# Performance work log

Measured on AMD Instinct MI355X. Metric: run time of the kernel, lower is better.

## Reference

```python
import jax, jax.numpy as jnp
import numpy as np

N, E = 50000, 800000
IN_F, HID, OUT, HEADS = 128, 64, 128, 4
NEG_SLOPE = 0.2


def setup_inputs() -> dict:
    key = jax.random.key(0)
    ks = jax.random.split(key, 10)
    s = 0.05
    return {
        "x": jax.random.normal(ks[0], (N, IN_F), dtype=jnp.float32),
        "edge_index": jax.random.randint(ks[1], (2, E), 0, N, dtype=jnp.int64),
        "W1": jax.random.normal(ks[2], (IN_F, HEADS * HID), dtype=jnp.float32) * s,
        "att_src1": jax.random.normal(ks[3], (HEADS, HID), dtype=jnp.float32) * s,
        "att_dst1": jax.random.normal(ks[4], (HEADS, HID), dtype=jnp.float32) * s,
        "b1": jnp.zeros((HEADS * HID,), dtype=jnp.float32),
        "W2": jax.random.normal(ks[5], (HEADS * HID, OUT), dtype=jnp.float32) * s,
        "att_src2": jax.random.normal(ks[6], (1, OUT), dtype=jnp.float32) * s,
        "att_dst2": jax.random.normal(ks[7], (1, OUT), dtype=jnp.float32) * s,
        "b2": jnp.zeros((OUT,), dtype=jnp.float32),
    }


def _gat_layer(x, W, a_src, a_dst, b, src, dst, heads, out_c):
    n = x.shape[0]
    h = (x @ W).reshape(n, heads, out_c)              # [N, H, C]
    alpha_s = jnp.einsum("nhc,hc->nh", h, a_src)       # [N, H]
    alpha_d = jnp.einsum("nhc,hc->nh", h, a_dst)
    e = jax.nn.leaky_relu(alpha_s[src] + alpha_d[dst], NEG_SLOPE)  # [E, H]
    # scatter-softmax over edges grouped by destination node
    m = jax.ops.segment_max(e, dst, num_segments=n)
    ex = jnp.exp(e - m[dst])
    denom = jax.ops.segment_sum(ex, dst, num_segments=n)
    alpha = ex / denom[dst]                            # [E, H]
    out = jax.ops.segment_sum(alpha[:, :, None] * h[src], dst, num_segments=n)
    return out.reshape(n, heads * out_c) + b


def reference(x, edge_index, W1, att_src1, att_dst1, b1, W2, att_src2, att_dst2, b2):
    n = x.shape[0]
    loop = jnp.arange(n, dtype=edge_index.dtype)       # PyG add_self_loops=True
    src = jnp.concatenate([edge_index[0], loop])
    dst = jnp.concatenate([edge_index[1], loop])
    h = _gat_layer(x, W1, att_src1, att_dst1, b1, src, dst, HEADS, HID)
    h = jax.nn.elu(h)
    out = _gat_layer(h, W2, att_src2, att_dst2, b2, src, dst, 1, OUT)
    return out
```

## Files before the change

kernel.cpp:

```cpp
#include <hip/hip_runtime.h>
#include <hip/hip_bf16.h>

#define NEG_SLOPE 0.2f

typedef short bf16x8 __attribute__((ext_vector_type(8)));
typedef float f32x4 __attribute__((ext_vector_type(4)));

__device__ __forceinline__ float bf2f(unsigned short u) {
    return __uint_as_float(((unsigned int)u) << 16);
}
__device__ __forceinline__ unsigned short f2bf(float f) {
    unsigned int x = __float_as_uint(f);
    unsigned int lsb = (x >> 16) & 1u;
    x += 0x7fffu + lsb;
    return (unsigned short)(x >> 16);
}


__global__ void cast_x_kernel(const float* __restrict__ x, unsigned short* __restrict__ xb,
                              int n4) {
    int i = blockIdx.x * 256 + threadIdx.x;
    if (i >= n4) return;
    float4 v = *(const float4*)(x + (size_t)i * 4);
    ushort4 b;
    b.x = f2bf(v.x); b.y = f2bf(v.y); b.z = f2bf(v.z); b.w = f2bf(v.w);
    *(ushort4*)(xb + (size_t)i * 4) = b;
}

__global__ void cast_w_kernel(const float* __restrict__ W, unsigned short* __restrict__ Wt,
                              int K, int NC) {
    int idx = blockIdx.x * 256 + threadIdx.x;
    if (idx >= K * NC) return;
    int k = idx / NC, n = idx % NC;
    Wt[(size_t)n * K + k] = f2bf(W[idx]);
}


__global__ void degree_kernel(const int* __restrict__ ei, int E, int N,
                              int* __restrict__ deg) {
    int e = blockIdx.x * blockDim.x + threadIdx.x;
    int EA = E + N;
    if (e >= EA) return;
    int dst = (e < E) ? ei[E + e] : (e - E);
    atomicAdd(&deg[dst], 1);
}

__global__ void scan_local(const int* __restrict__ deg, int* __restrict__ offs,
                           int* __restrict__ bsum, int N) {
    __shared__ int wsum[16];
    int tid = threadIdx.x;
    int lane = tid & 63;
    int wave = tid >> 6;
    int i = blockIdx.x * 1024 + tid;
    int v = (i < N) ? deg[i] : 0;
    int x = v;
    #pragma unroll
    for (int off = 1; off < 64; off <<= 1) {
        int t = __shfl_up(x, off);
        if (lane >= off) x += t;
    }
    if (lane == 63) wsum[wave] = x;
    __syncthreads();
    if (wave == 0 && lane < 16) {
        int w = wsum[lane];
        #pragma unroll
        for (int off = 1; off < 16; off <<= 1) {
            int t = __shfl_up(w, off);
            if (lane >= off) w += t;
        }
        wsum[lane] = w;
    }
    __syncthreads();
    int wexcl = (wave > 0) ? wsum[wave - 1] : 0;
    if (i <= N) offs[i] = wexcl + x - v;
    if (tid == 0) bsum[blockIdx.x] = wsum[15];
}

__global__ void scan_bsums(int* __restrict__ bsum, int nb) {
    __shared__ int wsum[16];
    int tid = threadIdx.x;
    int lane = tid & 63;
    int wave = tid >> 6;
    int v = (tid < nb) ? bsum[tid] : 0;
    int x = v;
    #pragma unroll
    for (int off = 1; off < 64; off <<= 1) {
        int t = __shfl_up(x, off);
        if (lane >= off) x += t;
    }
    if (lane == 63) wsum[wave] = x;
    __syncthreads();
    if (wave == 0 && lane < 16) {
        int w = wsum[lane];
        #pragma unroll
        for (int off = 1; off < 16; off <<= 1) {
            int t = __shfl_up(w, off);
            if (lane >= off) w += t;
        }
        wsum[lane] = w;
    }
    __syncthreads();
    int wexcl = (wave > 0) ? wsum[wave - 1] : 0;
    if (tid < nb) bsum[tid] = wexcl + x - v;
}

__global__ void scan_add(int* __restrict__ offs, const int* __restrict__ bsum, int N) {
    int i = blockIdx.x * 1024 + threadIdx.x;
    if (i <= N) offs[i] += bsum[blockIdx.x];
}

__global__ void scatter_kernel(const int* __restrict__ ei, int E, int N,
                               const int* __restrict__ offs, int* __restrict__ cnt,
                               int* __restrict__ col) {
    int e = blockIdx.x * blockDim.x + threadIdx.x;
    int EA = E + N;
    if (e >= EA) return;
    int s, d;
    if (e < E) { s = ei[e]; d = ei[E + e]; }
    else       { s = d = e - E; }
    int pos = offs[d] + atomicAdd(&cnt[d], 1);
    col[pos] = s;
}

__global__ void gemm1_mfma(const unsigned short* __restrict__ Ab,
                           const unsigned short* __restrict__ Wt,
                           unsigned short* __restrict__ hb, int M) {
    int wave = threadIdx.x >> 6;
    int lane = threadIdx.x & 63;
    int quad = lane >> 4;
    int l16 = lane & 15;
    int m0 = blockIdx.x * 64 + wave * 16;
    int rowc = min(m0 + l16, M - 1);
    bf16x8 a[4];
    const unsigned short* ap = Ab + (size_t)rowc * 128 + quad * 8;
    #pragma unroll
    for (int kc = 0; kc < 4; ++kc) a[kc] = *(const bf16x8*)(ap + kc * 32);
    f32x4 acc[16];
    #pragma unroll
    for (int nt = 0; nt < 16; ++nt) {
        f32x4 c = {0.f, 0.f, 0.f, 0.f};
        const unsigned short* bp = Wt + (size_t)(nt * 16 + l16) * 128 + quad * 8;
        #pragma unroll
        for (int kc = 0; kc < 4; ++kc) {
            bf16x8 b = *(const bf16x8*)(bp + kc * 32);
            c = __builtin_amdgcn_mfma_f32_16x16x32_bf16(a[kc], b, c, 0, 0, 0);
        }
        acc[nt] = c;
    }
    int srow0 = m0 + quad * 4;
    #pragma unroll
    for (int r = 0; r < 4; ++r) {
        int srow = srow0 + r;
        if (srow < M) {
            #pragma unroll
            for (int nt = 0; nt < 16; ++nt)
                hb[(size_t)srow * 256 + nt * 16 + l16] = f2bf(acc[nt][r]);
        }
    }
}

__global__ void gemm2_mfma(const unsigned short* __restrict__ Ab,
                           const unsigned short* __restrict__ Wt,
                           unsigned short* __restrict__ hb, int M) {
    int wave = threadIdx.x >> 6;
    int lane = threadIdx.x & 63;
    int quad = lane >> 4;
    int l16 = lane & 15;
    int m0 = blockIdx.x * 64 + wave * 16;
    int rowc = min(m0 + l16, M - 1);
    bf16x8 a[8];
    const unsigned short* ap = Ab + (size_t)rowc * 256 + quad * 8;
    #pragma unroll
    for (int kc = 0; kc < 8; ++kc) a[kc] = *(const bf16x8*)(ap + kc * 32);
    f32x4 acc[8];
    #pragma unroll
    for (int nt = 0; nt < 8; ++nt) {
        f32x4 c = {0.f, 0.f, 0.f, 0.f};
        const unsigned short* bp = Wt + (size_t)(nt * 16 + l16) * 256 + quad * 8;
        #pragma unroll
        for (int kc = 0; kc < 8; ++kc) {
            bf16x8 b = *(const bf16x8*)(bp + kc * 32);
            c = __builtin_amdgcn_mfma_f32_16x16x32_bf16(a[kc], b, c, 0, 0, 0);
        }
        acc[nt] = c;
    }
    int srow0 = m0 + quad * 4;
    #pragma unroll
    for (int r = 0; r < 4; ++r) {
        int srow = srow0 + r;
        if (srow < M) {
            #pragma unroll
            for (int nt = 0; nt < 8; ++nt)
                hb[(size_t)srow * 128 + nt * 16 + l16] = f2bf(acc[nt][r]);
        }
    }
}

__global__ void alpha1_kernel(const unsigned short* __restrict__ hb,
                              const float* __restrict__ att_s,
                              const float* __restrict__ att_d,
                              float* __restrict__ as, float* __restrict__ ad, int N) {
    int node = blockIdx.x * 4 + (threadIdx.x >> 6);
    if (node >= N) return;
    int lane = threadIdx.x & 63;
    int c0 = lane * 4;
    uint2 g = *(const uint2*)(hb + (size_t)node * 256 + c0);
    float h0 = __uint_as_float(g.x << 16);
    float h1 = __uint_as_float(g.x & 0xffff0000u);
    float h2 = __uint_as_float(g.y << 16);
    float h3 = __uint_as_float(g.y & 0xffff0000u);
    float4 sv = *(const float4*)(att_s + c0);
    float4 dv = *(const float4*)(att_d + c0);
    float ps = h0 * sv.x + h1 * sv.y + h2 * sv.z + h3 * sv.w;
    float pd = h0 * dv.x + h1 * dv.y + h2 * dv.z + h3 * dv.w;
    #pragma unroll
    for (int off = 1; off < 16; off <<= 1) {
        ps += __shfl_xor(ps, off);
        pd += __shfl_xor(pd, off);
    }
    if ((lane & 15) == 0) {
        int head = lane >> 4;
        as[node * 4 + head] = ps;
        ad[node * 4 + head] = pd;
    }
}

__global__ void alpha2_kernel(const unsigned short* __restrict__ hb,
                              const float* __restrict__ att_s,
                              const float* __restrict__ att_d,
                              float* __restrict__ as, float* __restrict__ ad, int N) {
    int node = blockIdx.x * 4 + (threadIdx.x >> 6);
    if (node >= N) return;
    int lane = threadIdx.x & 63;
    int c0 = lane * 2;
    unsigned int g = *(const unsigned int*)(hb + (size_t)node * 128 + c0);
    float h0 = __uint_as_float(g << 16);
    float h1 = __uint_as_float(g & 0xffff0000u);
    float2 sv = *(const float2*)(att_s + c0);
    float2 dv = *(const float2*)(att_d + c0);
    float ps = h0 * sv.x + h1 * sv.y;
    float pd = h0 * dv.x + h1 * dv.y;
    #pragma unroll
    for (int off = 1; off < 64; off <<= 1) {
        ps += __shfl_xor(ps, off);
        pd += __shfl_xor(pd, off);
    }
    if (lane == 0) { as[node] = ps; ad[node] = pd; }
}

__global__ void agg1_kernel(const unsigned short* __restrict__ hb,
                            const float* __restrict__ as,
                            const float* __restrict__ ad,
                            const int* __restrict__ offs, const int* __restrict__ col,
                            const float* __restrict__ b1,
                            unsigned short* __restrict__ out, int N) {
    int node = blockIdx.x * 4 + (threadIdx.x >> 6);
    if (node >= N) return;
    int lane = threadIdx.x & 63;
    int half = lane >> 5;
    int sub  = lane & 31;
    int head = sub >> 3;
    int c0 = sub * 8;
    float adv = ad[node * 4 + head];
    int beg = offs[node], end = offs[node + 1];
    float d = 0.f;
    float acc[8] = {};
    int j = beg + half;
    for (; j + 2 < end; j += 4) {
        int s0 = col[j];
        int s1 = col[j + 2];
        uint4 g0 = *(const uint4*)(hb + (size_t)s0 * 256 + c0);
        uint4 g1 = *(const uint4*)(hb + (size_t)s1 * 256 + c0);
        float e0 = as[s0 * 4 + head] + adv;
        float e1 = as[s1 * 4 + head] + adv;
        e0 = (e0 > 0.f) ? e0 : NEG_SLOPE * e0;
        e1 = (e1 > 0.f) ? e1 : NEG_SLOPE * e1;
        float p0 = __expf(e0);
        float p1 = __expf(e1);
        d += p0 + p1;
        const unsigned int* w0 = (const unsigned int*)&g0;
        const unsigned int* w1 = (const unsigned int*)&g1;
        #pragma unroll
        for (int i = 0; i < 4; ++i) {
            acc[2 * i]     = fmaf(p0, __uint_as_float(w0[i] << 16), acc[2 * i]);
            acc[2 * i + 1] = fmaf(p0, __uint_as_float(w0[i] & 0xffff0000u), acc[2 * i + 1]);
            acc[2 * i]     = fmaf(p1, __uint_as_float(w1[i] << 16), acc[2 * i]);
            acc[2 * i + 1] = fmaf(p1, __uint_as_float(w1[i] & 0xffff0000u), acc[2 * i + 1]);
        }
    }
    for (; j < end; j += 2) {
        int s = col[j];
        uint4 g = *(const uint4*)(hb + (size_t)s * 256 + c0);
        float e = as[s * 4 + head] + adv;
        e = (e > 0.f) ? e : NEG_SLOPE * e;
        float p = __expf(e);
        d += p;
        const unsigned int* w = (const unsigned int*)&g;
        #pragma unroll
        for (int i = 0; i < 4; ++i) {
            acc[2 * i]     = fmaf(p, __uint_as_float(w[i] << 16), acc[2 * i]);
            acc[2 * i + 1] = fmaf(p, __uint_as_float(w[i] & 0xffff0000u), acc[2 * i + 1]);
        }
    }
    d += __shfl_xor(d, 32);
    #pragma unroll
    for (int i = 0; i < 8; ++i) acc[i] += __shfl_xor(acc[i], 32);
    if (half == 0) {
        float inv = 1.f / d;
        float4 bb0 = *(const float4*)(b1 + c0);
        float4 bb1 = *(const float4*)(b1 + c0 + 4);
        float bb[8] = {bb0.x, bb0.y, bb0.z, bb0.w, bb1.x, bb1.y, bb1.z, bb1.w};
        unsigned short o[8];
        #pragma unroll
        for (int i = 0; i < 8; ++i) {
            float v = acc[i] * inv + bb[i];
            v = (v > 0.f) ? v : (__expf(v) - 1.f);
            o[i] = f2bf(v);
        }
        ushort4 p0 = {o[0], o[1], o[2], o[3]};
        ushort4 p1 = {o[4], o[5], o[6], o[7]};
        *(ushort4*)(out + (size_t)node * 256 + c0) = p0;
        *(ushort4*)(out + (size_t)node * 256 + c0 + 4) = p1;
    }
}

__global__ void agg2_kernel(const unsigned short* __restrict__ hb,
                            const float* __restrict__ as,
                            const float* __restrict__ ad,
                            const int* __restrict__ offs, const int* __restrict__ col,
                            const float* __restrict__ b2,
                            float* __restrict__ out, int N) {
    int node = blockIdx.x * 4 + (threadIdx.x >> 6);
    if (node >= N) return;
    int lane = threadIdx.x & 63;
    int q   = lane >> 4;
    int sub = lane & 15;
    int c0 = sub * 8;
    float adv = ad[node];
    int beg = offs[node], end = offs[node + 1];
    float d = 0.f;
    float acc[8] = {};
    int j = beg + q;
    for (; j + 4 < end; j += 8) {
        int s0 = col[j];
        int s1 = col[j + 4];
        uint4 g0 = *(const uint4*)(hb + (size_t)s0 * 128 + c0);
        uint4 g1 = *(const uint4*)(hb + (size_t)s1 * 128 + c0);
        float e0 = as[s0] + adv;
        float e1 = as[s1] + adv;
        e0 = (e0 > 0.f) ? e0 : NEG_SLOPE * e0;
        e1 = (e1 > 0.f) ? e1 : NEG_SLOPE * e1;
        float p0 = __expf(e0);
        float p1 = __expf(e1);
        d += p0 + p1;
        const unsigned int* w0 = (const unsigned int*)&g0;
        const unsigned int* w1 = (const unsigned int*)&g1;
        #pragma unroll
        for (int i = 0; i < 4; ++i) {
            acc[2 * i]     = fmaf(p0, __uint_as_float(w0[i] << 16), acc[2 * i]);
            acc[2 * i + 1] = fmaf(p0, __uint_as_float(w0[i] & 0xffff0000u), acc[2 * i + 1]);
            acc[2 * i]     = fmaf(p1, __uint_as_float(w1[i] << 16), acc[2 * i]);
            acc[2 * i + 1] = fmaf(p1, __uint_as_float(w1[i] & 0xffff0000u), acc[2 * i + 1]);
        }
    }
    for (; j < end; j += 4) {
        int s = col[j];
        uint4 g = *(const uint4*)(hb + (size_t)s * 128 + c0);
        float e = as[s] + adv;
        e = (e > 0.f) ? e : NEG_SLOPE * e;
        float p = __expf(e);
        d += p;
        const unsigned int* w = (const unsigned int*)&g;
        #pragma unroll
        for (int i = 0; i < 4; ++i) {
            acc[2 * i]     = fmaf(p, __uint_as_float(w[i] << 16), acc[2 * i]);
            acc[2 * i + 1] = fmaf(p, __uint_as_float(w[i] & 0xffff0000u), acc[2 * i + 1]);
        }
    }
    d += __shfl_xor(d, 16);
    d += __shfl_xor(d, 32);
    #pragma unroll
    for (int i = 0; i < 8; ++i) {
        acc[i] += __shfl_xor(acc[i], 16);
        acc[i] += __shfl_xor(acc[i], 32);
    }
    if (lane < 16) {
        float inv = 1.f / d;
        float4 bb0 = *(const float4*)(b2 + c0);
        float4 bb1 = *(const float4*)(b2 + c0 + 4);
        float bb[8] = {bb0.x, bb0.y, bb0.z, bb0.w, bb1.x, bb1.y, bb1.z, bb1.w};
        float o[8];
        #pragma unroll
        for (int i = 0; i < 8; ++i) o[i] = acc[i] * inv + bb[i];
        *(float4*)(out + (size_t)node * 128 + c0) = make_float4(o[0], o[1], o[2], o[3]);
        *(float4*)(out + (size_t)node * 128 + c0 + 4) = make_float4(o[4], o[5], o[6], o[7]);
    }
}


extern "C" void kernel_launch(void* const* d_in, const int* in_sizes, int n_in,
                              void* d_out, int out_size, void* d_ws, size_t ws_size,
                              hipStream_t stream) {
    const float* x    = (const float*)d_in[0];
    const int*   ei   = (const int*)d_in[1];
    const float* W1   = (const float*)d_in[2];
    const float* at_s1 = (const float*)d_in[3];
    const float* at_d1 = (const float*)d_in[4];
    const float* b1   = (const float*)d_in[5];
    const float* W2   = (const float*)d_in[6];
    const float* at_s2 = (const float*)d_in[7];
    const float* at_d2 = (const float*)d_in[8];
    const float* b2   = (const float*)d_in[9];
    float* out = (float*)d_out;

    const int N  = in_sizes[0] / 128;
    const int E  = in_sizes[1] / 2;
    const int EA = E + N;

    char* ws = (char*)d_ws;
    size_t off = 0;
    auto alloc = [&](size_t bytes) -> void* {
        void* p = ws + off;
        off += (bytes + 255) & ~(size_t)255;
        return p;
    };
    unsigned short* xb   = (unsigned short*)alloc((size_t)N * 128 * 2);
    unsigned short* wt1  = (unsigned short*)alloc((size_t)256 * 128 * 2);
    unsigned short* wt2  = (unsigned short*)alloc((size_t)128 * 256 * 2);
    unsigned short* h1b  = (unsigned short*)alloc((size_t)N * 256 * 2);
    unsigned short* h1ab = (unsigned short*)alloc((size_t)N * 256 * 2);
    unsigned short* h2b  = (unsigned short*)alloc((size_t)N * 128 * 2);
    float* as1 = (float*)alloc((size_t)N * 4 * 4);
    float* ad1 = (float*)alloc((size_t)N * 4 * 4);
    float* as2 = (float*)alloc((size_t)N * 4);
    float* ad2 = (float*)alloc((size_t)N * 4);
    int* deg  = (int*)alloc((size_t)2 * N * 4);
    int* cnt  = deg + N;
    int* offs = (int*)alloc((size_t)(N + 1) * 4);
    int* bsum = (int*)alloc((size_t)1024 * 4);
    int* col  = (int*)alloc((size_t)EA * 4);

    const int nb = (N + 1 + 1023) / 1024;

    hipMemsetAsync(deg, 0, (size_t)2 * N * 4, stream);
    cast_x_kernel<<<(N * 128 / 4 + 255) / 256, 256, 0, stream>>>(x, xb, N * 128 / 4);
    cast_w_kernel<<<(128 * 256 + 255) / 256, 256, 0, stream>>>(W1, wt1, 128, 256);
    cast_w_kernel<<<(256 * 128 + 255) / 256, 256, 0, stream>>>(W2, wt2, 256, 128);
    degree_kernel<<<(EA + 255) / 256, 256, 0, stream>>>(ei, E, N, deg);
    scan_local<<<nb, 1024, 0, stream>>>(deg, offs, bsum, N);
    scan_bsums<<<1, 1024, 0, stream>>>(bsum, nb);
    scan_add<<<nb, 1024, 0, stream>>>(offs, bsum, N);
    scatter_kernel<<<(EA + 255) / 256, 256, 0, stream>>>(ei, E, N, offs, cnt, col);

    gemm1_mfma<<<(N + 63) / 64, 256, 0, stream>>>(xb, wt1, h1b, N);
    alpha1_kernel<<<(N + 3) / 4, 256, 0, stream>>>(h1b, at_s1, at_d1, as1, ad1, N);
    agg1_kernel<<<(N + 3) / 4, 256, 0, stream>>>(h1b, as1, ad1, offs, col, b1, h1ab, N);

    gemm2_mfma<<<(N + 63) / 64, 256, 0, stream>>>(h1ab, wt2, h2b, N);
    alpha2_kernel<<<(N + 3) / 4, 256, 0, stream>>>(h2b, at_s2, at_d2, as2, ad2, N);
    agg2_kernel<<<(N + 3) / 4, 256, 0, stream>>>(h2b, as2, ad2, offs, col, b2, out, N);
}
```

Baseline: 371.5 us.

## Fuse x cast and attention-score dots into GEMM epilogues; unroll aggregation

```diff
diff --git a/kernel.cpp b/kernel.cpp
--- a/kernel.cpp
+++ b/kernel.cpp
@@ -5,6 +5,7 @@
 
 typedef short bf16x8 __attribute__((ext_vector_type(8)));
 typedef float f32x4 __attribute__((ext_vector_type(4)));
+typedef float f32x2 __attribute__((ext_vector_type(2)));
 
 __device__ __forceinline__ float bf2f(unsigned short u) {
     return __uint_as_float(((unsigned int)u) << 16);
@@ -15,16 +16,11 @@
     x += 0x7fffu + lsb;
     return (unsigned short)(x >> 16);
 }
-
-
-__global__ void cast_x_kernel(const float* __restrict__ x, unsigned short* __restrict__ xb,
-                              int n4) {
-    int i = blockIdx.x * 256 + threadIdx.x;
-    if (i >= n4) return;
-    float4 v = *(const float4*)(x + (size_t)i * 4);
-    ushort4 b;
-    b.x = f2bf(v.x); b.y = f2bf(v.y); b.z = f2bf(v.z); b.w = f2bf(v.w);
-    *(ushort4*)(xb + (size_t)i * 4) = b;
+__device__ __forceinline__ f32x2 upk(unsigned int u) {
+    f32x2 r;
+    r.x = __uint_as_float(u << 16);
+    r.y = __uint_as_float(u & 0xffff0000u);
+    return r;
 }
 
 __global__ void cast_w_kernel(const float* __restrict__ W, unsigned short* __restrict__ Wt,
@@ -122,9 +118,11 @@
     col[pos] = s;
 }
 
-__global__ void gemm1_mfma(const unsigned short* __restrict__ Ab,
+__global__ void gemm1_mfma(const float* __restrict__ A,
                            const unsigned short* __restrict__ Wt,
-                           unsigned short* __restrict__ hb, int M) {
+                           const float* __restrict__ att_s, const float* __restrict__ att_d,
+                           unsigned short* __restrict__ hb,
+                           float* __restrict__ as, float* __restrict__ ad, int M) {
     int wave = threadIdx.x >> 6;
     int lane = threadIdx.x & 63;
     int quad = lane >> 4;
@@ -132,9 +130,18 @@
     int m0 = blockIdx.x * 64 + wave * 16;
     int rowc = min(m0 + l16, M - 1);
     bf16x8 a[4];
-    const unsigned short* ap = Ab + (size_t)rowc * 128 + quad * 8;
-    #pragma unroll
-    for (int kc = 0; kc < 4; ++kc) a[kc] = *(const bf16x8*)(ap + kc * 32);
+    const float* ap = A + (size_t)rowc * 128 + quad * 8;
+    #pragma unroll
+    for (int kc = 0; kc < 4; ++kc) {
+        float4 f0 = *(const float4*)(ap + kc * 32);
+        float4 f1 = *(const float4*)(ap + kc * 32 + 4);
+        bf16x8 v;
+        v[0] = (short)f2bf(f0.x); v[1] = (short)f2bf(f0.y);
+        v[2] = (short)f2bf(f0.z); v[3] = (short)f2bf(f0.w);
+        v[4] = (short)f2bf(f1.x); v[5] = (short)f2bf(f1.y);
+        v[6] = (short)f2bf(f1.z); v[7] = (short)f2bf(f1.w);
+        a[kc] = v;
+    }
     f32x4 acc[16];
     #pragma unroll
     for (int nt = 0; nt < 16; ++nt) {
@@ -147,21 +154,46 @@
         }
         acc[nt] = c;
     }
+    float asv[16], adv[16];
+    #pragma unroll
+    for (int nt = 0; nt < 16; ++nt) {
+        asv[nt] = att_s[nt * 16 + l16];
+        adv[nt] = att_d[nt * 16 + l16];
+    }
     int srow0 = m0 + quad * 4;
     #pragma unroll
     for (int r = 0; r < 4; ++r) {
         int srow = srow0 + r;
-        if (srow < M) {
+        bool ok = srow < M;
+        if (ok) {
             #pragma unroll
             for (int nt = 0; nt < 16; ++nt)
                 hb[(size_t)srow * 256 + nt * 16 + l16] = f2bf(acc[nt][r]);
         }
+        #pragma unroll
+        for (int h = 0; h < 4; ++h) {
+            float ps = acc[4 * h][r] * asv[4 * h] + acc[4 * h + 1][r] * asv[4 * h + 1]
+                     + acc[4 * h + 2][r] * asv[4 * h + 2] + acc[4 * h + 3][r] * asv[4 * h + 3];
+            float pd = acc[4 * h][r] * adv[4 * h] + acc[4 * h + 1][r] * adv[4 * h + 1]
+                     + acc[4 * h + 2][r] * adv[4 * h + 2] + acc[4 * h + 3][r] * adv[4 * h + 3];
+            #pragma unroll
+            for (int off = 1; off < 16; off <<= 1) {
+                ps += __shfl_xor(ps, off);
+                pd += __shfl_xor(pd, off);
+            }
+            if (ok && l16 == 0) {
+                as[srow * 4 + h] = ps;
+                ad[srow * 4 + h] = pd;
+            }
+        }
     }
 }
 
 __global__ void gemm2_mfma(const unsigned short* __restrict__ Ab,
                            const unsigned short* __restrict__ Wt,
-                           unsigned short* __restrict__ hb, int M) {
+                           const float* __restrict__ att_s, const float* __restrict__ att_d,
+                           unsigned short* __restrict__ hb,
+                           float* __restrict__ as, float* __restrict__ ad, int M) {
     int wave = threadIdx.x >> 6;
     int lane = threadIdx.x & 63;
     int quad = lane >> 4;
@@ -184,68 +216,35 @@
         }
         acc[nt] = c;
     }
+    float asv[8], adv[8];
+    #pragma unroll
+    for (int nt = 0; nt < 8; ++nt) {
+        asv[nt] = att_s[nt * 16 + l16];
+        adv[nt] = att_d[nt * 16 + l16];
+    }
     int srow0 = m0 + quad * 4;
     #pragma unroll
     for (int r = 0; r < 4; ++r) {
         int srow = srow0 + r;
-        if (srow < M) {
+        bool ok = srow < M;
+        if (ok) {
             #pragma unroll
             for (int nt = 0; nt < 8; ++nt)
                 hb[(size_t)srow * 128 + nt * 16 + l16] = f2bf(acc[nt][r]);
         }
-    }
-}
-
-__global__ void alpha1_kernel(const unsigned short* __restrict__ hb,
-                              const float* __restrict__ att_s,
-                              const float* __restrict__ att_d,
-                              float* __restrict__ as, float* __restrict__ ad, int N) {
-    int node = blockIdx.x * 4 + (threadIdx.x >> 6);
-    if (node >= N) return;
-    int lane = threadIdx.x & 63;
-    int c0 = lane * 4;
-    uint2 g = *(const uint2*)(hb + (size_t)node * 256 + c0);
-    float h0 = __uint_as_float(g.x << 16);
-    float h1 = __uint_as_float(g.x & 0xffff0000u);
-    float h2 = __uint_as_float(g.y << 16);
-    float h3 = __uint_as_float(g.y & 0xffff0000u);
-    float4 sv = *(const float4*)(att_s + c0);
-    float4 dv = *(const float4*)(att_d + c0);
-    float ps = h0 * sv.x + h1 * sv.y + h2 * sv.z + h3 * sv.w;
-    float pd = h0 * dv.x + h1 * dv.y + h2 * dv.z + h3 * dv.w;
-    #pragma unroll
-    for (int off = 1; off < 16; off <<= 1) {
-        ps += __shfl_xor(ps, off);
-        pd += __shfl_xor(pd, off);
-    }
-    if ((lane & 15) == 0) {
-        int head = lane >> 4;
-        as[node * 4 + head] = ps;
-        ad[node * 4 + head] = pd;
-    }
-}
-
-__global__ void alpha2_kernel(const unsigned short* __restrict__ hb,
-                              const float* __restrict__ att_s,
-                              const float* __restrict__ att_d,
-                              float* __restrict__ as, float* __restrict__ ad, int N) {
-    int node = blockIdx.x * 4 + (threadIdx.x >> 6);
-    if (node >= N) return;
-    int lane = threadIdx.x & 63;
-    int c0 = lane * 2;
-    unsigned int g = *(const unsigned int*)(hb + (size_t)node * 128 + c0);
-    float h0 = __uint_as_float(g << 16);
-    float h1 = __uint_as_float(g & 0xffff0000u);
-    float2 sv = *(const float2*)(att_s + c0);
-    float2 dv = *(const float2*)(att_d + c0);
-    float ps = h0 * sv.x + h1 * sv.y;
-    float pd = h0 * dv.x + h1 * dv.y;
-    #pragma unroll
-    for (int off = 1; off < 64; off <<= 1) {
-        ps += __shfl_xor(ps, off);
-        pd += __shfl_xor(pd, off);
-    }
-    if (lane == 0) { as[node] = ps; ad[node] = pd; }
+        float ps = 0.f, pd = 0.f;
+        #pragma unroll
+        for (int nt = 0; nt < 8; ++nt) {
+            ps = fmaf(acc[nt][r], asv[nt], ps);
+            pd = fmaf(acc[nt][r], adv[nt], pd);
+        }
+        #pragma unroll
+        for (int off = 1; off < 16; off <<= 1) {
+            ps += __shfl_xor(ps, off);
+            pd += __shfl_xor(pd, off);
+        }
+        if (ok && l16 == 0) { as[srow] = ps; ad[srow] = pd; }
+    }
 }
 
 __global__ void agg1_kernel(const unsigned short* __restrict__ hb,
@@ -264,8 +263,40 @@
     float adv = ad[node * 4 + head];
     int beg = offs[node], end = offs[node + 1];
     float d = 0.f;
-    float acc[8] = {};
+    f32x2 acc[4] = {};
     int j = beg + half;
+    for (; j + 6 < end; j += 8) {
+        int s0 = col[j];
+        int s1 = col[j + 2];
+        int s2 = col[j + 4];
+        int s3 = col[j + 6];
+        uint4 g0 = *(const uint4*)(hb + (size_t)s0 * 256 + c0);
+        uint4 g1 = *(const uint4*)(hb + (size_t)s1 * 256 + c0);
+        uint4 g2 = *(const uint4*)(hb + (size_t)s2 * 256 + c0);
+        uint4 g3 = *(const uint4*)(hb + (size_t)s3 * 256 + c0);
+        float e0 = as[s0 * 4 + head] + adv;
+        float e1 = as[s1 * 4 + head] + adv;
+        float e2 = as[s2 * 4 + head] + adv;
+        float e3 = as[s3 * 4 + head] + adv;
+        e0 = (e0 > 0.f) ? e0 : NEG_SLOPE * e0;
+        e1 = (e1 > 0.f) ? e1 : NEG_SLOPE * e1;
+        e2 = (e2 > 0.f) ? e2 : NEG_SLOPE * e2;
+        e3 = (e3 > 0.f) ? e3 : NEG_SLOPE * e3;
+        float p0 = __expf(e0), p1 = __expf(e1), p2 = __expf(e2), p3 = __expf(e3);
+        d += (p0 + p1) + (p2 + p3);
+        const unsigned int* w0 = (const unsigned int*)&g0;
+        const unsigned int* w1 = (const unsigned int*)&g1;
+        const unsigned int* w2 = (const unsigned int*)&g2;
+        const unsigned int* w3 = (const unsigned int*)&g3;
+        f32x2 v0 = {p0, p0}, v1 = {p1, p1}, v2 = {p2, p2}, v3 = {p3, p3};
+        #pragma unroll
+        for (int i = 0; i < 4; ++i) {
+            acc[i] = __builtin_elementwise_fma(v0, upk(w0[i]), acc[i]);
+            acc[i] = __builtin_elementwise_fma(v1, upk(w1[i]), acc[i]);
+            acc[i] = __builtin_elementwise_fma(v2, upk(w2[i]), acc[i]);
+            acc[i] = __builtin_elementwise_fma(v3, upk(w3[i]), acc[i]);
+        }
+    }
     for (; j + 2 < end; j += 4) {
         int s0 = col[j];
         int s1 = col[j + 2];
@@ -275,17 +306,15 @@
         float e1 = as[s1 * 4 + head] + adv;
         e0 = (e0 > 0.f) ? e0 : NEG_SLOPE * e0;
         e1 = (e1 > 0.f) ? e1 : NEG_SLOPE * e1;
-        float p0 = __expf(e0);
-        float p1 = __expf(e1);
+        float p0 = __expf(e0), p1 = __expf(e1);
         d += p0 + p1;
         const unsigned int* w0 = (const unsigned int*)&g0;
         const unsigned int* w1 = (const unsigned int*)&g1;
+        f32x2 v0 = {p0, p0}, v1 = {p1, p1};
         #pragma unroll
         for (int i = 0; i < 4; ++i) {
-            acc[2 * i]     = fmaf(p0, __uint_as_float(w0[i] << 16), acc[2 * i]);
-            acc[2 * i + 1] = fmaf(p0, __uint_as_float(w0[i] & 0xffff0000u), acc[2 * i + 1]);
-            acc[2 * i]     = fmaf(p1, __uint_as_float(w1[i] << 16), acc[2 * i]);
-            acc[2 * i + 1] = fmaf(p1, __uint_as_float(w1[i] & 0xffff0000u), acc[2 * i + 1]);
+            acc[i] = __builtin_elementwise_fma(v0, upk(w0[i]), acc[i]);
+            acc[i] = __builtin_elementwise_fma(v1, upk(w1[i]), acc[i]);
         }
     }
     for (; j < end; j += 2) {
@@ -296,24 +325,28 @@
         float p = __expf(e);
         d += p;
         const unsigned int* w = (const unsigned int*)&g;
-        #pragma unroll
-        for (int i = 0; i < 4; ++i) {
-            acc[2 * i]     = fmaf(p, __uint_as_float(w[i] << 16), acc[2 * i]);
-            acc[2 * i + 1] = fmaf(p, __uint_as_float(w[i] & 0xffff0000u), acc[2 * i + 1]);
-        }
+        f32x2 v = {p, p};
+        #pragma unroll
+        for (int i = 0; i < 4; ++i)
+            acc[i] = __builtin_elementwise_fma(v, upk(w[i]), acc[i]);
     }
     d += __shfl_xor(d, 32);
     #pragma unroll
-    for (int i = 0; i < 8; ++i) acc[i] += __shfl_xor(acc[i], 32);
+    for (int i = 0; i < 4; ++i) {
+        acc[i].x += __shfl_xor(acc[i].x, 32);
+        acc[i].y += __shfl_xor(acc[i].y, 32);
+    }
     if (half == 0) {
         float inv = 1.f / d;
         float4 bb0 = *(const float4*)(b1 + c0);
         float4 bb1 = *(const float4*)(b1 + c0 + 4);
+        float av[8] = {acc[0].x, acc[0].y, acc[1].x, acc[1].y,
+                       acc[2].x, acc[2].y, acc[3].x, acc[3].y};
         float bb[8] = {bb0.x, bb0.y, bb0.z, bb0.w, bb1.x, bb1.y, bb1.z, bb1.w};
         unsigned short o[8];
         #pragma unroll
         for (int i = 0; i < 8; ++i) {
-            float v = acc[i] * inv + bb[i];
+            float v = av[i] * inv + bb[i];
             v = (v > 0.f) ? v : (__expf(v) - 1.f);
             o[i] = f2bf(v);
         }
@@ -339,7 +372,7 @@
     float adv = ad[node];
     int beg = offs[node], end = offs[node + 1];
     float d = 0.f;
-    float acc[8] = {};
+    f32x2 acc[4] = {};
     int j = beg + q;
     for (; j + 4 < end; j += 8) {
         int s0 = col[j];
@@ -350,17 +383,15 @@
         float e1 = as[s1] + adv;
         e0 = (e0 > 0.f) ? e0 : NEG_SLOPE * e0;
         e1 = (e1 > 0.f) ? e1 : NEG_SLOPE * e1;
-        float p0 = __expf(e0);
-        float p1 = __expf(e1);
+        float p0 = __expf(e0), p1 = __expf(e1);
         d += p0 + p1;
         const unsigned int* w0 = (const unsigned int*)&g0;
         const unsigned int* w1 = (const unsigned int*)&g1;
+        f32x2 v0 = {p0, p0}, v1 = {p1, p1};
         #pragma unroll
         for (int i = 0; i < 4; ++i) {
-            acc[2 * i]     = fmaf(p0, __uint_as_float(w0[i] << 16), acc[2 * i]);
-            acc[2 * i + 1] = fmaf(p0, __uint_as_float(w0[i] & 0xffff0000u), acc[2 * i + 1]);
-            acc[2 * i]     = fmaf(p1, __uint_as_float(w1[i] << 16), acc[2 * i]);
-            acc[2 * i + 1] = fmaf(p1, __uint_as_float(w1[i] & 0xffff0000u), acc[2 * i + 1]);
+            acc[i] = __builtin_elementwise_fma(v0, upk(w0[i]), acc[i]);
+            acc[i] = __builtin_elementwise_fma(v1, upk(w1[i]), acc[i]);
         }
     }
     for (; j < end; j += 4) {
@@ -371,27 +402,30 @@
         float p = __expf(e);
         d += p;
         const unsigned int* w = (const unsigned int*)&g;
-        #pragma unroll
-        for (int i = 0; i < 4; ++i) {
-            acc[2 * i]     = fmaf(p, __uint_as_float(w[i] << 16), acc[2 * i]);
-            acc[2 * i + 1] = fmaf(p, __uint_as_float(w[i] & 0xffff0000u), acc[2 * i + 1]);
-        }
+        f32x2 v = {p, p};
+        #pragma unroll
+        for (int i = 0; i < 4; ++i)
+            acc[i] = __builtin_elementwise_fma(v, upk(w[i]), acc[i]);
     }
     d += __shfl_xor(d, 16);
     d += __shfl_xor(d, 32);
     #pragma unroll
-    for (int i = 0; i < 8; ++i) {
-        acc[i] += __shfl_xor(acc[i], 16);
-        acc[i] += __shfl_xor(acc[i], 32);
+    for (int i = 0; i < 4; ++i) {
+        acc[i].x += __shfl_xor(acc[i].x, 16);
+        acc[i].x += __shfl_xor(acc[i].x, 32);
+        acc[i].y += __shfl_xor(acc[i].y, 16);
+        acc[i].y += __shfl_xor(acc[i].y, 32);
     }
     if (lane < 16) {
         float inv = 1.f / d;
         float4 bb0 = *(const float4*)(b2 + c0);
         float4 bb1 = *(const float4*)(b2 + c0 + 4);
+        float av[8] = {acc[0].x, acc[0].y, acc[1].x, acc[1].y,
+                       acc[2].x, acc[2].y, acc[3].x, acc[3].y};
         float bb[8] = {bb0.x, bb0.y, bb0.z, bb0.w, bb1.x, bb1.y, bb1.z, bb1.w};
         float o[8];
         #pragma unroll
-        for (int i = 0; i < 8; ++i) o[i] = acc[i] * inv + bb[i];
+        for (int i = 0; i < 8; ++i) o[i] = av[i] * inv + bb[i];
         *(float4*)(out + (size_t)node * 128 + c0) = make_float4(o[0], o[1], o[2], o[3]);
         *(float4*)(out + (size_t)node * 128 + c0 + 4) = make_float4(o[4], o[5], o[6], o[7]);
     }
@@ -424,7 +458,6 @@
         off += (bytes + 255) & ~(size_t)255;
         return p;
     };
-    unsigned short* xb   = (unsigned short*)alloc((size_t)N * 128 * 2);
     unsigned short* wt1  = (unsigned short*)alloc((size_t)256 * 128 * 2);
     unsigned short* wt2  = (unsigned short*)alloc((size_t)128 * 256 * 2);
     unsigned short* h1b  = (unsigned short*)alloc((size_t)N * 256 * 2);
@@ -443,7 +476,6 @@
     const int nb = (N + 1 + 1023) / 1024;
 
     hipMemsetAsync(deg, 0, (size_t)2 * N * 4, stream);
-    cast_x_kernel<<<(N * 128 / 4 + 255) / 256, 256, 0, stream>>>(x, xb, N * 128 / 4);
     cast_w_kernel<<<(128 * 256 + 255) / 256, 256, 0, stream>>>(W1, wt1, 128, 256);
     cast_w_kernel<<<(256 * 128 + 255) / 256, 256, 0, stream>>>(W2, wt2, 256, 128);
     degree_kernel<<<(EA + 255) / 256, 256, 0, stream>>>(ei, E, N, deg);
@@ -452,11 +484,9 @@
     scan_add<<<nb, 1024, 0, stream>>>(offs, bsum, N);
     scatter_kernel<<<(EA + 255) / 256, 256, 0, stream>>>(ei, E, N, offs, cnt, col);
 
-    gemm1_mfma<<<(N + 63) / 64, 256, 0, stream>>>(xb, wt1, h1b, N);
-    alpha1_kernel<<<(N + 3) / 4, 256, 0, stream>>>(h1b, at_s1, at_d1, as1, ad1, N);
+    gemm1_mfma<<<(N + 63) / 64, 256, 0, stream>>>(x, wt1, at_s1, at_d1, h1b, as1, ad1, N);
     agg1_kernel<<<(N + 3) / 4, 256, 0, stream>>>(h1b, as1, ad1, offs, col, b1, h1ab, N);
 
-    gemm2_mfma<<<(N + 63) / 64, 256, 0, stream>>>(h1ab, wt2, h2b, N);
-    alpha2_kernel<<<(N + 3) / 4, 256, 0, stream>>>(h2b, at_s2, at_d2, as2, ad2, N);
+    gemm2_mfma<<<(N + 63) / 64, 256, 0, stream>>>(h1ab, wt2, at_s2, at_d2, h2b, as2, ad2, N);
     agg2_kernel<<<(N + 3) / 4, 256, 0, stream>>>(h2b, as2, ad2, offs, col, b2, out, N);
 }
```

After: 351.6 us. -5.4%, faster.
